# Kernel optimization log

Hardware: AMD Instinct MI355X
Metric: run time of the kernel (lower is better)

Reference implementation:

```python
import jax, jax.numpy as jnp
import numpy as np

N = 8192
IN_F = 512
OUT_F = 512
ALPHA = 0.2  # leaky relu slope


def setup_inputs() -> dict:
    key = jax.random.key(0)
    k1, k2, k3, k4, k5 = jax.random.split(key, 5)
    inp = jax.random.normal(k1, (N, IN_F), dtype=jnp.float32)
    adj = jax.random.randint(k2, (N, N), 0, 2, dtype=jnp.int32)
    # linear1: [in, out] + bias
    W1 = jax.random.normal(k3, (IN_F, OUT_F), dtype=jnp.float32) * (1.0 / np.sqrt(IN_F))
    b1 = jnp.zeros((OUT_F,), dtype=jnp.float32)
    # linear2: maps 2*out -> 1; split into the two halves acting on h_i and h_j
    a = jax.random.normal(k4, (2 * OUT_F,), dtype=jnp.float32) * (1.0 / np.sqrt(2 * OUT_F))
    a1 = a[:OUT_F]
    a2 = a[OUT_F:]
    b2 = jnp.zeros((), dtype=jnp.float32)
    return {"inp": inp, "adj": adj, "W1": W1, "b1": b1, "a1": a1, "a2": a2, "b2": b2}


def reference(inp, adj, W1, b1, a1, a2, b2):
    h = inp @ W1 + b1  # [N, out]
    # linear2(cat(h_i, h_j)) == h_i@a1 + h_j@a2 + b2 -> avoids the N*N*2F tensor
    e = jax.nn.leaky_relu((h @ a1)[:, None] + (h @ a2)[None, :] + b2, ALPHA)  # [N, N]
    attention = jnp.where(adj > 0, e, jnp.float32(-1e12))
    attention = jax.nn.softmax(attention, axis=1)
    h_prime = attention @ h  # [N, out]
    return jax.nn.elu(h_prime)  # concat=True
```

## Files before the change

kernel.cpp:

```cpp
#include <hip/hip_runtime.h>
#include <hip/hip_bf16.h>
#include <stdint.h>

#define NR 8192
#define FD 512
#define BM 64

typedef __attribute__((ext_vector_type(8))) short s8v;
typedef __attribute__((ext_vector_type(4))) float f32x4;

static __device__ __forceinline__ short bf16_rtne(float x) {
    union { float f; uint32_t u; } v; v.f = x;
    uint32_t r = (v.u + 0x7FFFu + ((v.u >> 16) & 1u)) >> 16;
    return (short)r;
}
static __device__ __forceinline__ float bf16_to_f32(short s) {
    union { uint32_t u; float f; } v; v.u = ((uint32_t)(uint16_t)s) << 16;
    return v.f;
}

__global__ void k_prep(const float* __restrict__ in, short* __restrict__ out,
                       const float* __restrict__ W1, short* __restrict__ W1T) {
    int b = blockIdx.x;
    if (b < 4096) {
        int i = b * 256 + threadIdx.x;
        float4 v = ((const float4*)in)[i];
        short4 s;
        s.x = bf16_rtne(v.x); s.y = bf16_rtne(v.y);
        s.z = bf16_rtne(v.z); s.w = bf16_rtne(v.w);
        ((short4*)out)[i] = s;
    } else {
        int i = (b - 4096) * 256 + threadIdx.x;
        int k = i & 511, n = i >> 9;
        W1T[(size_t)n * 512 + k] = bf16_rtne(W1[(size_t)k * 512 + n]);
    }
}

__launch_bounds__(256)
__global__ void k_gemm_h(const short* __restrict__ A,
                         const short* __restrict__ BT,
                         const float* __restrict__ b1,
                         short* __restrict__ H,
                         short* __restrict__ HT3)
{
    const int lane = threadIdx.x & 63;
    const int wn   = threadIdx.x >> 6;
    const int m    = lane & 15;
    const int q    = lane >> 4;
    const int r0   = blockIdx.x * 32;
    const int c0   = blockIdx.y * 128 + wn * 32;

    f32x4 acc[2][2] = {};
#pragma unroll 1
    for (int k0 = 0; k0 < 512; k0 += 32) {
        s8v a[2], b[2];
#pragma unroll
        for (int rt = 0; rt < 2; ++rt)
            a[rt] = *(const s8v*)(A + (size_t)(r0 + rt * 16 + m) * 512 + k0 + q * 8);
#pragma unroll
        for (int nt = 0; nt < 2; ++nt)
            b[nt] = *(const s8v*)(BT + (size_t)(c0 + nt * 16 + m) * 512 + k0 + q * 8);
#pragma unroll
        for (int rt = 0; rt < 2; ++rt)
#pragma unroll
            for (int nt = 0; nt < 2; ++nt)
                acc[rt][nt] = __builtin_amdgcn_mfma_f32_16x16x32_bf16(a[rt], b[nt], acc[rt][nt], 0, 0, 0);
    }
    float b1v[2];
#pragma unroll
    for (int nt = 0; nt < 2; ++nt) b1v[nt] = b1[c0 + nt * 16 + m];

#pragma unroll
    for (int rt = 0; rt < 2; ++rt)
#pragma unroll
        for (int nt = 0; nt < 2; ++nt) {
            int col = c0 + nt * 16 + m;
            short4 hp;
#pragma unroll
            for (int r = 0; r < 4; ++r) {
                int row = r0 + rt * 16 + q * 4 + r;
                short hv = bf16_rtne(acc[rt][nt][r] + b1v[nt]);
                H[(size_t)row * 512 + col] = hv;
                ((short*)&hp)[r] = hv;
            }
            size_t off = (size_t)blockIdx.x * 16384
                       + (size_t)(blockIdx.y * 2 + (wn >> 1)) * 2048
                       + (size_t)((wn * 2 + nt) & 3) * 512
                       + (rt * 2 + (q >> 1)) * 128
                       + m * 8 + (q & 1) * 4;
            *(short4*)(HT3 + off) = hp;
        }
}

__global__ void k_f1f2(const short* __restrict__ H, const float* __restrict__ a1,
                       const float* __restrict__ a2, const float* __restrict__ b2,
                       float* __restrict__ f1, float* __restrict__ f2s)
{
    const int lane = threadIdx.x & 63;
    const int row  = blockIdx.x * 4 + (threadIdx.x >> 6);
    s8v hv = *(const s8v*)(H + (size_t)row * 512 + lane * 8);
    float4 a1l = ((const float4*)(a1 + lane * 8))[0];
    float4 a1h = ((const float4*)(a1 + lane * 8))[1];
    float4 a2l = ((const float4*)(a2 + lane * 8))[0];
    float4 a2h = ((const float4*)(a2 + lane * 8))[1];
    float hf[8];
#pragma unroll
    for (int i = 0; i < 8; ++i) hf[i] = bf16_to_f32(hv[i]);
    float s1 = hf[0] * a1l.x + hf[1] * a1l.y + hf[2] * a1l.z + hf[3] * a1l.w
             + hf[4] * a1h.x + hf[5] * a1h.y + hf[6] * a1h.z + hf[7] * a1h.w;
    float s2 = hf[0] * a2l.x + hf[1] * a2l.y + hf[2] * a2l.z + hf[3] * a2l.w
             + hf[4] * a2h.x + hf[5] * a2h.y + hf[6] * a2h.z + hf[7] * a2h.w;
#pragma unroll
    for (int o = 32; o > 0; o >>= 1) {
        s1 += __shfl_xor(s1, o);
        s2 += __shfl_xor(s2, o);
    }
    if (lane == 0) {
        f1[row]  = s1;
        f2s[row] = s2 + b2[0];
    }
}

__launch_bounds__(512, 2)
__global__ void k_attn(const int* __restrict__ adj,
                       const short* __restrict__ HT3,
                       const float* __restrict__ f1,
                       const float* __restrict__ f2s,
                       float* __restrict__ nump,
                       float* __restrict__ denomp)
{
    __shared__ __align__(16) short wt[2][BM * 256];

    const int t    = threadIdx.x;
    const int lane = t & 63;
    const int w    = t >> 6;
    const int m    = lane & 15;
    const int q    = lane >> 4;

    const int js   = blockIdx.x & 1;
    const int band = blockIdx.x >> 1;
    const int r0   = band * BM;
    const int jb0  = js * 4096;
    const int jt0  = js * 128;

    const int prow = t >> 3;
    const int jg   = t & 7;

    const float f1v = f1[r0 + prow];
    const int* adjrow = adj + (size_t)(r0 + prow) * NR + jb0;
    const float* f2base = f2s + jb0;

    f32x4 acc[4][4] = {};
    float dsum = 0.f;

#define GAT_BLOAD(DST, KT)                                                     \
    {                                                                          \
        const short* s_ = HT3 + (size_t)(jt0 + (KT)) * 16384 + w * 2048        \
                        + q * 128 + m * 8;                                     \
        DST[0] = *(const s8v*)(s_);                                            \
        DST[1] = *(const s8v*)(s_ + 512);                                      \
        DST[2] = *(const s8v*)(s_ + 1024);                                     \
        DST[3] = *(const s8v*)(s_ + 1536);                                     \
    }

#define GAT_MLOAD(DST, AP, U)                                                  \
    {                                                                          \
        uint4 ma_ = *(const uint4*)((AP) + (U) * 8);                           \
        uint4 mb_ = *(const uint4*)((AP) + (U) * 8 + 4);                       \
        DST = ((int)ma_.x > 0 ? 1u : 0u)  | ((int)ma_.y > 0 ? 2u : 0u)         \
            | ((int)ma_.z > 0 ? 4u : 0u)  | ((int)ma_.w > 0 ? 8u : 0u)         \
            | ((int)mb_.x > 0 ? 16u : 0u) | ((int)mb_.y > 0 ? 32u : 0u)        \
            | ((int)mb_.z > 0 ? 64u : 0u) | ((int)mb_.w > 0 ? 128u : 0u);      \
    }

#define GAT_WUNIT(U, BYTE, FA, FB, P)                                          \
    {                                                                          \
        s8v wv_;                                                               \
        const float* ff_ = (const float*)&(FA);                                \
        _Pragma("unroll")                                                      \
        for (int jj = 0; jj < 4; ++jj) {                                       \
            float s_ = f1v + ff_[jj];                                          \
            float e_ = __expf(fmaxf(s_, 0.2f * s_));                           \
            float x_ = (((BYTE) >> jj) & 1u) ? e_ : 0.f;                       \
            dsum += x_; wv_[jj] = bf16_rtne(x_);                               \
        }                                                                      \
        const float* fg_ = (const float*)&(FB);                               \
        _Pragma("unroll")                                                      \
        for (int jj = 0; jj < 4; ++jj) {                                       \
            float s_ = f1v + fg_[jj];                                          \
            float e_ = __expf(fmaxf(s_, 0.2f * s_));                           \
            float x_ = (((BYTE) >> (4 + jj)) & 1u) ? e_ : 0.f;                 \
            dsum += x_; wv_[4 + jj] = bf16_rtne(x_);                           \
        }                                                                      \
        *(s8v*)&wt[P][prow * 256 + (((U) ^ (prow & 7)) << 3)] = wv_;           \
    }

    {
#pragma unroll
        for (int k_ = 0; k_ < 4; ++k_) {
            const int u_ = jg + 8 * k_;
            uint32_t mk_;
            GAT_MLOAD(mk_, adjrow, u_)
            float4 fa_ = *(const float4*)(f2base + u_ * 8);
            float4 fb_ = *(const float4*)(f2base + u_ * 8 + 4);
            GAT_WUNIT(u_, mk_, fa_, fb_, 0)
        }
    }
    s8v breg[2][4];
    GAT_BLOAD(breg[0], 0)
    GAT_BLOAD(breg[1], 1)
    __syncthreads();

    int kt = 0;
#pragma unroll 1
    for (int ch = 0; ch < 16; ++ch) {
        const int p = ch & 1;
        const int chn = (ch + 1) & 15;
        const int* adjn = adjrow + chn * 256;
        const float* f2n = f2base + chn * 256;
        uint32_t mkn_[4];
        float4 fan_[4], fbn_[4];

#pragma unroll
        for (int kk = 0; kk < 8; ++kk, ++kt) {
            const int e = kk & 1;
            s8v bn[4];
            GAT_BLOAD(bn, (kt + 2) & 127)
            if (kk < 4 && ch < 15) {
                const int u_ = jg + 8 * kk;
                GAT_MLOAD(mkn_[kk], adjn, u_)
                fan_[kk] = *(const float4*)(f2n + u_ * 8);
                fbn_[kk] = *(const float4*)(f2n + u_ * 8 + 4);
            }
            s8v af[4];
#pragma unroll
            for (int i = 0; i < 4; ++i)
                af[i] = *(const s8v*)&wt[p][(i * 16 + m) * 256
                                            + (((kk * 4 + q) ^ (m & 7)) << 3)];
#pragma unroll
            for (int nt = 0; nt < 4; ++nt)
#pragma unroll
                for (int i = 0; i < 4; ++i)
                    acc[i][nt] = __builtin_amdgcn_mfma_f32_16x16x32_bf16(af[i], breg[e][nt], acc[i][nt], 0, 0, 0);
            if (kk >= 3 && kk <= 6 && ch < 15) {
                const int k_ = kk - 3;
                const int u_ = jg + 8 * k_;
                GAT_WUNIT(u_, mkn_[k_], fan_[k_], fbn_[k_], p ^ 1)
            }
#pragma unroll
            for (int nt = 0; nt < 4; ++nt) breg[e][nt] = bn[nt];
        }
        __syncthreads();
    }
#undef GAT_BLOAD
#undef GAT_MLOAD
#undef GAT_WUNIT

    dsum += __shfl_xor(dsum, 1);
    dsum += __shfl_xor(dsum, 2);
    dsum += __shfl_xor(dsum, 4);
    if (jg == 0) denomp[(size_t)js * NR + r0 + prow] = dsum;

    float* np = nump + (size_t)js * NR * FD;
#pragma unroll
    for (int i = 0; i < 4; ++i)
#pragma unroll
        for (int nt = 0; nt < 4; ++nt)
#pragma unroll
            for (int r = 0; r < 4; ++r) {
                int row = r0 + i * 16 + q * 4 + r;
                int col = w * 64 + nt * 16 + m;
                np[(size_t)row * FD + col] = acc[i][nt][r];
            }
}

__global__ void k_combine(const float* __restrict__ nump,
                          const float* __restrict__ denomp,
                          float* __restrict__ out)
{
    size_t e = ((size_t)blockIdx.x * 256 + threadIdx.x) * 4;
    int row = (int)(e >> 9);
    float4 n0 = *(const float4*)(nump + e);
    float4 n1 = *(const float4*)(nump + (size_t)NR * FD + e);
    float d = denomp[row] + denomp[NR + row];
    float inv = 1.0f / d;
    float4 o;
    o.x = (n0.x + n1.x) * inv;
    o.y = (n0.y + n1.y) * inv;
    o.z = (n0.z + n1.z) * inv;
    o.w = (n0.w + n1.w) * inv;
    o.x = (o.x > 0.f) ? o.x : (__expf(o.x) - 1.f);
    o.y = (o.y > 0.f) ? o.y : (__expf(o.y) - 1.f);
    o.z = (o.z > 0.f) ? o.z : (__expf(o.z) - 1.f);
    o.w = (o.w > 0.f) ? o.w : (__expf(o.w) - 1.f);
    *(float4*)(out + e) = o;
}

extern "C" void kernel_launch(void* const* d_in, const int* in_sizes, int n_in,
                              void* d_out, int out_size, void* d_ws, size_t ws_size,
                              hipStream_t stream) {
    const float* inp = (const float*)d_in[0];
    const int*   adj = (const int*)d_in[1];
    const float* W1  = (const float*)d_in[2];
    const float* b1  = (const float*)d_in[3];
    const float* a1  = (const float*)d_in[4];
    const float* a2  = (const float*)d_in[5];
    const float* b2  = (const float*)d_in[6];
    float* out = (float*)d_out;

    short*    inp_bf = (short*)d_ws;
    short*    w1t    = inp_bf + (size_t)NR * FD;
    short*    h      = w1t + (size_t)FD * FD;
    short*    ht3    = h + (size_t)NR * FD;
    float*    f1     = (float*)(ht3 + (size_t)FD * NR);
    float*    f2s    = f1 + NR;
    float*    nump   = f2s + NR;
    float*    denomp = nump + (size_t)2 * NR * FD;

    k_prep<<<4096 + 1024, 256, 0, stream>>>(inp, inp_bf, W1, w1t);
    dim3 g1(NR / 32, FD / 128);
    k_gemm_h<<<g1, 256, 0, stream>>>(inp_bf, w1t, b1, h, ht3);
    k_f1f2<<<NR / 4, 256, 0, stream>>>(h, a1, a2, b2, f1, f2s);
    k_attn<<<128 * 2, 512, 0, stream>>>(adj, ht3, f1, f2s, nump, denomp);
    k_combine<<<(NR * FD / 4) / 256, 256, 0, stream>>>(nump, denomp, out);
}
```

Measured before the change: 486.1 us.

## Split attention kernel into producer and consumer warp groups

The block grows to 1024 threads and becomes warp-specialized. Eight producer waves load the adjacency mask and f2, compute the masked exp weights, write them to the double-buffered shared tile, and accumulate the denominator. The other eight consumer waves only issue the MFMA tiles against H. This replaces the manual software pipelining that interleaved both jobs in the same waves. In exchange, launch_bounds(1024,4) caps the registers available to each thread, which can cause spills of the 64 accumulator registers. The B-register prefetch depth also drops from two steps to one.

Result: slower. 512.5 us (+5.4%).

```diff
diff --git a/kernel.cpp b/kernel.cpp
--- a/kernel.cpp
+++ b/kernel.cpp
@@ -121,7 +121,7 @@
     }
 }
 
-__launch_bounds__(512, 2)
+__launch_bounds__(1024, 4)
 __global__ void k_attn(const int* __restrict__ adj,
                        const short* __restrict__ HT3,
                        const float* __restrict__ f1,
@@ -133,7 +133,7 @@
 
     const int t    = threadIdx.x;
     const int lane = t & 63;
-    const int w    = t >> 6;
+    const int wv   = t >> 6;
     const int m    = lane & 15;
     const int q    = lane >> 4;
 
@@ -143,19 +143,9 @@
     const int jb0  = js * 4096;
     const int jt0  = js * 128;
 
-    const int prow = t >> 3;
-    const int jg   = t & 7;
-
-    const float f1v = f1[r0 + prow];
-    const int* adjrow = adj + (size_t)(r0 + prow) * NR + jb0;
-    const float* f2base = f2s + jb0;
-
-    f32x4 acc[4][4] = {};
-    float dsum = 0.f;
-
 #define GAT_BLOAD(DST, KT)                                                     \
     {                                                                          \
-        const short* s_ = HT3 + (size_t)(jt0 + (KT)) * 16384 + w * 2048        \
+        const short* s_ = HT3 + (size_t)(jt0 + (KT)) * 16384 + wv * 2048       \
                         + q * 128 + m * 8;                                     \
         DST[0] = *(const s8v*)(s_);                                            \
         DST[1] = *(const s8v*)(s_ + 512);                                      \
@@ -163,115 +153,112 @@
         DST[3] = *(const s8v*)(s_ + 1536);                                     \
     }
 
-#define GAT_MLOAD(DST, AP, U)                                                  \
+#define GAT_WUNIT(U, AP, FP, P)                                                \
     {                                                                          \
         uint4 ma_ = *(const uint4*)((AP) + (U) * 8);                           \
         uint4 mb_ = *(const uint4*)((AP) + (U) * 8 + 4);                       \
-        DST = ((int)ma_.x > 0 ? 1u : 0u)  | ((int)ma_.y > 0 ? 2u : 0u)         \
-            | ((int)ma_.z > 0 ? 4u : 0u)  | ((int)ma_.w > 0 ? 8u : 0u)         \
-            | ((int)mb_.x > 0 ? 16u : 0u) | ((int)mb_.y > 0 ? 32u : 0u)        \
-            | ((int)mb_.z > 0 ? 64u : 0u) | ((int)mb_.w > 0 ? 128u : 0u);      \
-    }
-
-#define GAT_WUNIT(U, BYTE, FA, FB, P)                                          \
-    {                                                                          \
+        float4 fa_ = *(const float4*)((FP) + (U) * 8);                         \
+        float4 fb_ = *(const float4*)((FP) + (U) * 8 + 4);                     \
+        uint32_t bm_ =                                                         \
+              ((int)ma_.x > 0 ? 1u : 0u)   | ((int)ma_.y > 0 ? 2u : 0u)        \
+            | ((int)ma_.z > 0 ? 4u : 0u)   | ((int)ma_.w > 0 ? 8u : 0u)        \
+            | ((int)mb_.x > 0 ? 16u : 0u)  | ((int)mb_.y > 0 ? 32u : 0u)       \
+            | ((int)mb_.z > 0 ? 64u : 0u)  | ((int)mb_.w > 0 ? 128u : 0u);     \
         s8v wv_;                                                               \
-        const float* ff_ = (const float*)&(FA);                                \
+        const float* ff_ = (const float*)&fa_;                                 \
         _Pragma("unroll")                                                      \
         for (int jj = 0; jj < 4; ++jj) {                                       \
             float s_ = f1v + ff_[jj];                                          \
             float e_ = __expf(fmaxf(s_, 0.2f * s_));                           \
-            float x_ = (((BYTE) >> jj) & 1u) ? e_ : 0.f;                       \
+            float x_ = ((bm_ >> jj) & 1u) ? e_ : 0.f;                          \
             dsum += x_; wv_[jj] = bf16_rtne(x_);                               \
         }                                                                      \
-        const float* fg_ = (const float*)&(FB);                               \
+        const float* fg_ = (const float*)&fb_;                                 \
         _Pragma("unroll")                                                      \
         for (int jj = 0; jj < 4; ++jj) {                                       \
             float s_ = f1v + fg_[jj];                                          \
             float e_ = __expf(fmaxf(s_, 0.2f * s_));                           \
-            float x_ = (((BYTE) >> (4 + jj)) & 1u) ? e_ : 0.f;                 \
+            float x_ = ((bm_ >> (4 + jj)) & 1u) ? e_ : 0.f;                    \
             dsum += x_; wv_[4 + jj] = bf16_rtne(x_);                           \
         }                                                                      \
         *(s8v*)&wt[P][prow * 256 + (((U) ^ (prow & 7)) << 3)] = wv_;           \
     }
 
-    {
-#pragma unroll
-        for (int k_ = 0; k_ < 4; ++k_) {
-            const int u_ = jg + 8 * k_;
-            uint32_t mk_;
-            GAT_MLOAD(mk_, adjrow, u_)
-            float4 fa_ = *(const float4*)(f2base + u_ * 8);
-            float4 fb_ = *(const float4*)(f2base + u_ * 8 + 4);
-            GAT_WUNIT(u_, mk_, fa_, fb_, 0)
+    if (wv >= 8) {
+        const int ptid = t - 512;
+        const int prow = ptid >> 3;
+        const int jg   = ptid & 7;
+        const float f1v = f1[r0 + prow];
+        const int* adjrow = adj + (size_t)(r0 + prow) * NR + jb0;
+        const float* f2base = f2s + jb0;
+        float dsum = 0.f;
+
+#pragma unroll
+        for (int k_ = 0; k_ < 4; ++k_)
+            GAT_WUNIT(jg + 8 * k_, adjrow, f2base, 0)
+        __syncthreads();
+
+#pragma unroll 1
+        for (int ch = 0; ch < 16; ++ch) {
+            if (ch < 15) {
+                const int* ap = adjrow + (ch + 1) * 256;
+                const float* fp = f2base + (ch + 1) * 256;
+                const int pn = (ch + 1) & 1;
+#pragma unroll
+                for (int k_ = 0; k_ < 4; ++k_)
+                    GAT_WUNIT(jg + 8 * k_, ap, fp, pn)
+            }
+            __syncthreads();
         }
-    }
-    s8v breg[2][4];
-    GAT_BLOAD(breg[0], 0)
-    GAT_BLOAD(breg[1], 1)
-    __syncthreads();
-
-    int kt = 0;
+
+        dsum += __shfl_xor(dsum, 1);
+        dsum += __shfl_xor(dsum, 2);
+        dsum += __shfl_xor(dsum, 4);
+        if (jg == 0) denomp[(size_t)js * NR + r0 + prow] = dsum;
+    } else {
+        f32x4 acc[4][4] = {};
+        s8v breg[4];
+        GAT_BLOAD(breg, 0)
+        __syncthreads();
+
+        int kt = 0;
 #pragma unroll 1
-    for (int ch = 0; ch < 16; ++ch) {
-        const int p = ch & 1;
-        const int chn = (ch + 1) & 15;
-        const int* adjn = adjrow + chn * 256;
-        const float* f2n = f2base + chn * 256;
-        uint32_t mkn_[4];
-        float4 fan_[4], fbn_[4];
-
-#pragma unroll
-        for (int kk = 0; kk < 8; ++kk, ++kt) {
-            const int e = kk & 1;
-            s8v bn[4];
-            GAT_BLOAD(bn, (kt + 2) & 127)
-            if (kk < 4 && ch < 15) {
-                const int u_ = jg + 8 * kk;
-                GAT_MLOAD(mkn_[kk], adjn, u_)
-                fan_[kk] = *(const float4*)(f2n + u_ * 8);
-                fbn_[kk] = *(const float4*)(f2n + u_ * 8 + 4);
+        for (int ch = 0; ch < 16; ++ch) {
+            const int p = ch & 1;
+#pragma unroll
+            for (int kk = 0; kk < 8; ++kk, ++kt) {
+                s8v bn[4];
+                GAT_BLOAD(bn, (kt + 1) & 127)
+                s8v af[4];
+#pragma unroll
+                for (int i = 0; i < 4; ++i)
+                    af[i] = *(const s8v*)&wt[p][(i * 16 + m) * 256
+                                                + (((kk * 4 + q) ^ (m & 7)) << 3)];
+#pragma unroll
+                for (int nt = 0; nt < 4; ++nt)
+#pragma unroll
+                    for (int i = 0; i < 4; ++i)
+                        acc[i][nt] = __builtin_amdgcn_mfma_f32_16x16x32_bf16(af[i], breg[nt], acc[i][nt], 0, 0, 0);
+#pragma unroll
+                for (int nt = 0; nt < 4; ++nt) breg[nt] = bn[nt];
             }
-            s8v af[4];
-#pragma unroll
-            for (int i = 0; i < 4; ++i)
-                af[i] = *(const s8v*)&wt[p][(i * 16 + m) * 256
-                                            + (((kk * 4 + q) ^ (m & 7)) << 3)];
+            __syncthreads();
+        }
+
+        float* np = nump + (size_t)js * NR * FD;
+#pragma unroll
+        for (int i = 0; i < 4; ++i)
 #pragma unroll
             for (int nt = 0; nt < 4; ++nt)
 #pragma unroll
-                for (int i = 0; i < 4; ++i)
-                    acc[i][nt] = __builtin_amdgcn_mfma_f32_16x16x32_bf16(af[i], breg[e][nt], acc[i][nt], 0, 0, 0);
-            if (kk >= 3 && kk <= 6 && ch < 15) {
-                const int k_ = kk - 3;
-                const int u_ = jg + 8 * k_;
-                GAT_WUNIT(u_, mkn_[k_], fan_[k_], fbn_[k_], p ^ 1)
-            }
-#pragma unroll
-            for (int nt = 0; nt < 4; ++nt) breg[e][nt] = bn[nt];
-        }
-        __syncthreads();
+                for (int r = 0; r < 4; ++r) {
+                    int row = r0 + i * 16 + q * 4 + r;
+                    int col = wv * 64 + nt * 16 + m;
+                    np[(size_t)row * FD + col] = acc[i][nt][r];
+                }
     }
 #undef GAT_BLOAD
-#undef GAT_MLOAD
 #undef GAT_WUNIT
-
-    dsum += __shfl_xor(dsum, 1);
-    dsum += __shfl_xor(dsum, 2);
-    dsum += __shfl_xor(dsum, 4);
-    if (jg == 0) denomp[(size_t)js * NR + r0 + prow] = dsum;
-
-    float* np = nump + (size_t)js * NR * FD;
-#pragma unroll
-    for (int i = 0; i < 4; ++i)
-#pragma unroll
-        for (int nt = 0; nt < 4; ++nt)
-#pragma unroll
-            for (int r = 0; r < 4; ++r) {
-                int row = r0 + i * 16 + q * 4 + r;
-                int col = w * 64 + nt * 16 + m;
-                np[(size_t)row * FD + col] = acc[i][nt][r];
-            }
 }
 
 __global__ void k_combine(const float* __restrict__ nump,
@@ -321,6 +308,6 @@
     dim3 g1(NR / 32, FD / 128);
     k_gemm_h<<<g1, 256, 0, stream>>>(inp_bf, w1t, b1, h, ht3);
     k_f1f2<<<NR / 4, 256, 0, stream>>>(h, a1, a2, b2, f1, f2s);
-    k_attn<<<128 * 2, 512, 0, stream>>>(adj, ht3, f1, f2s, nump, denomp);
+    k_attn<<<128 * 2, 1024, 0, stream>>>(adj, ht3, f1, f2s, nump, denomp);
     k_combine<<<(NR * FD / 4) / 256, 256, 0, stream>>>(nump, denomp, out);
 }
```
